# Kernel tuning notes

Hardware: AMD Instinct MI355X
Metric: run time of the kernel (lower is better)

Reference implementation:

```python
import jax, jax.numpy as jnp
import numpy as np

B, N, D, C = 256, 2000, 512, 100


def setup_inputs() -> dict:
    key = jax.random.key(0)
    k1, k2, k3, k4 = jax.random.split(key, 4)
    inputs = jax.random.normal(k1, (B, D), dtype=jnp.float32)
    support_tensors = jax.random.normal(k2, (N, D), dtype=jnp.float32)
    label_idx = jax.random.randint(k3, (N,), 0, C)
    support_labels = jax.nn.one_hot(label_idx, C, dtype=jnp.float32)
    kernel_w = jax.random.normal(k4, (D,), dtype=jnp.float32) * 0.05
    kernel_b = jnp.zeros((), dtype=jnp.float32)
    return {
        "inputs": inputs,
        "support_tensors": support_tensors,
        "support_labels": support_labels,
        "kernel_w": kernel_w,
        "kernel_b": kernel_b,
    }


def reference(inputs, support_tensors, support_labels, kernel_w, kernel_b):
    # Pairwise Cartesian product (batch x support): |a - b|, shape [B, N, D]
    diff = jnp.abs(inputs[:, None, :] - support_tensors[None, :, :])
    # Siamese kernel: sigmoid(Dense(1)(|a-b|)) -> scores [B, N]
    pair_wise_scores = jax.nn.sigmoid(jnp.einsum("bnd,d->bn", diff, kernel_w) + kernel_b)
    # Per-class aggregation: matmul with one-hot labels, then mean per class
    class_sums = pair_wise_scores @ support_labels  # [B, C]
    class_counts = jnp.sum(support_labels, axis=0)  # [C]
    # tf.math.divide_no_nan semantics
    return jnp.where(class_counts != 0, class_sums / class_counts, 0.0)
```

## Files before the change

kernel.cpp:

```cpp
#include <hip/hip_runtime.h>
#include <hip/hip_bf16.h>

#define B_SZ 256
#define N_SZ 2000
#define N_PAD 2048
#define D_SZ 512
#define C_SZ 100
#define BT 4
#define D4 (D_SZ / 4)
#define PF 4

__global__ void prep_kernel(const float* __restrict__ labels,
                            int* __restrict__ idx) {
    int n = blockIdx.x * 256 + threadIdx.x;
    if (n < N_SZ) {
        const float4* row = (const float4*)(labels + (size_t)n * C_SZ);
        int c = 0;
#pragma unroll
        for (int j = 0; j < C_SZ / 4; ++j) {
            float4 v = row[j];
            if (v.x > 0.5f) c = 4 * j + 0;
            if (v.y > 0.5f) c = 4 * j + 1;
            if (v.z > 0.5f) c = 4 * j + 2;
            if (v.w > 0.5f) c = 4 * j + 3;
        }
        idx[n] = c;
    }
}

__global__ void transpose_kernel(const float4* __restrict__ sup4,
                                 float4* __restrict__ supT4) {
    int t = blockIdx.x * 256 + threadIdx.x;
    int dc = t >> 11;
    int n  = t & (N_PAD - 1);
    float4 v = make_float4(0.f, 0.f, 0.f, 0.f);
    if (n < N_SZ) v = sup4[(size_t)n * D4 + dc];
    supT4[t] = v;
}

__global__ __launch_bounds__(256, 2) void score_kernel(
    const float4* __restrict__ inp4,
    const float4* __restrict__ supT4,
    const float4* __restrict__ w4,
    const float* __restrict__ bias_p,
    float* __restrict__ S)
{
    int tid = threadIdx.x;
    int n  = blockIdx.x * 256 + tid;
    int b0 = blockIdx.y * BT;

    const float4* __restrict__ a0 = inp4 + (size_t)(b0 + 0) * D4;
    const float4* __restrict__ a1 = inp4 + (size_t)(b0 + 1) * D4;
    const float4* __restrict__ a2 = inp4 + (size_t)(b0 + 2) * D4;
    const float4* __restrict__ a3 = inp4 + (size_t)(b0 + 3) * D4;

    const float4* __restrict__ sp = supT4 + n;

    float acc[BT] = {0.f, 0.f, 0.f, 0.f};

    auto compute = [&](int dc, const float4& sv) {
        float4 wv = w4[dc];
        float4 av;
        av = a0[dc];
        acc[0] += wv.x * fabsf(av.x - sv.x);
        acc[0] += wv.y * fabsf(av.y - sv.y);
        acc[0] += wv.z * fabsf(av.z - sv.z);
        acc[0] += wv.w * fabsf(av.w - sv.w);
        av = a1[dc];
        acc[1] += wv.x * fabsf(av.x - sv.x);
        acc[1] += wv.y * fabsf(av.y - sv.y);
        acc[1] += wv.z * fabsf(av.z - sv.z);
        acc[1] += wv.w * fabsf(av.w - sv.w);
        av = a2[dc];
        acc[2] += wv.x * fabsf(av.x - sv.x);
        acc[2] += wv.y * fabsf(av.y - sv.y);
        acc[2] += wv.z * fabsf(av.z - sv.z);
        acc[2] += wv.w * fabsf(av.w - sv.w);
        av = a3[dc];
        acc[3] += wv.x * fabsf(av.x - sv.x);
        acc[3] += wv.y * fabsf(av.y - sv.y);
        acc[3] += wv.z * fabsf(av.z - sv.z);
        acc[3] += wv.w * fabsf(av.w - sv.w);
    };

    float4 c0 = sp[(size_t)0 * N_PAD];
    float4 c1 = sp[(size_t)1 * N_PAD];
    float4 c2 = sp[(size_t)2 * N_PAD];
    float4 c3 = sp[(size_t)3 * N_PAD];

#pragma unroll 1
    for (int dc = 0; dc < D4 - PF; dc += PF) {
        float4 t0 = sp[(size_t)(dc + 4) * N_PAD];
        float4 t1 = sp[(size_t)(dc + 5) * N_PAD];
        float4 t2 = sp[(size_t)(dc + 6) * N_PAD];
        float4 t3 = sp[(size_t)(dc + 7) * N_PAD];
        compute(dc + 0, c0);
        compute(dc + 1, c1);
        compute(dc + 2, c2);
        compute(dc + 3, c3);
        c0 = t0; c1 = t1; c2 = t2; c3 = t3;
    }
    compute(D4 - 4, c0);
    compute(D4 - 3, c1);
    compute(D4 - 2, c2);
    compute(D4 - 1, c3);

    float bias = *bias_p;
#pragma unroll
    for (int i = 0; i < BT; ++i) {
        float s = 1.0f / (1.0f + __expf(-(acc[i] + bias)));
        S[(size_t)(b0 + i) * N_PAD + n] = s;
    }
}

__global__ void agg_kernel(const float* __restrict__ S,
                           const int* __restrict__ idx,
                           float* __restrict__ out) {
    __shared__ float sums[C_SZ];
    __shared__ float cnts[C_SZ];
    int b = blockIdx.x;
    int t = threadIdx.x;
    if (t < C_SZ) { sums[t] = 0.f; cnts[t] = 0.f; }
    __syncthreads();
    for (int n = t; n < N_SZ; n += 256) {
        int c = idx[n];
        atomicAdd(&sums[c], S[(size_t)b * N_PAD + n]);
        atomicAdd(&cnts[c], 1.0f);
    }
    __syncthreads();
    if (t < C_SZ) {
        float cnt = cnts[t];
        out[(size_t)b * C_SZ + t] = (cnt != 0.f) ? sums[t] / cnt : 0.f;
    }
}

extern "C" void kernel_launch(void* const* d_in, const int* in_sizes, int n_in,
                              void* d_out, int out_size, void* d_ws, size_t ws_size,
                              hipStream_t stream) {
    const float* inputs  = (const float*)d_in[0];
    const float* support = (const float*)d_in[1];
    const float* labels  = (const float*)d_in[2];
    const float* w       = (const float*)d_in[3];
    const float* bias    = (const float*)d_in[4];
    float* out = (float*)d_out;

    int*    idx   = (int*)d_ws;
    float4* supT4 = (float4*)((char*)d_ws + 16384);
    float*  S     = (float*)((char*)d_ws + 16384 + (size_t)D4 * N_PAD * sizeof(float4));

    prep_kernel<<<dim3((N_SZ + 255) / 256), dim3(256), 0, stream>>>(labels, idx);

    transpose_kernel<<<dim3(D4 * N_PAD / 256), dim3(256), 0, stream>>>(
        (const float4*)support, supT4);

    dim3 grid(N_PAD / 256, B_SZ / BT);
    score_kernel<<<grid, dim3(256), 0, stream>>>(
        (const float4*)inputs, supT4, (const float4*)w, bias, S);

    agg_kernel<<<dim3(B_SZ), dim3(256), 0, stream>>>(S, idx, out);
}
```

Baseline: 45.55 us.

## Split the D reduction across grid z and finish sigmoid in the aggregation kernel

The score kernel now splits the 512-wide feature reduction into four chunks along a third grid dimension. Each block writes partial logits to its own slice of the workspace, and the aggregation kernel adds the four partials plus the bias before applying the sigmoid. This multiplies the block count by four (from 512 blocks) and raises the launch-bounds occupancy hint, to fill the GPU better. In exchange it writes and reads four times as much intermediate data, and each block runs a much shorter loop with relatively more prologue overhead.

```diff
diff --git a/kernel.cpp b/kernel.cpp
--- a/kernel.cpp
+++ b/kernel.cpp
@@ -9,6 +9,8 @@
 #define BT 4
 #define D4 (D_SZ / 4)
 #define PF 4
+#define DSPLIT 4
+#define DQ (D4 / DSPLIT)
 
 __global__ void prep_kernel(const float* __restrict__ labels,
                             int* __restrict__ idx) {
@@ -38,28 +40,29 @@
     supT4[t] = v;
 }
 
-__global__ __launch_bounds__(256, 2) void score_kernel(
+__global__ __launch_bounds__(256, 8) void score_kernel(
     const float4* __restrict__ inp4,
     const float4* __restrict__ supT4,
     const float4* __restrict__ w4,
-    const float* __restrict__ bias_p,
     float* __restrict__ S)
 {
     int tid = threadIdx.x;
-    int n  = blockIdx.x * 256 + tid;
-    int b0 = blockIdx.y * BT;
+    int n   = blockIdx.x * 256 + tid;
+    int b0  = blockIdx.y * BT;
+    int off = blockIdx.z * DQ;
 
-    const float4* __restrict__ a0 = inp4 + (size_t)(b0 + 0) * D4;
-    const float4* __restrict__ a1 = inp4 + (size_t)(b0 + 1) * D4;
-    const float4* __restrict__ a2 = inp4 + (size_t)(b0 + 2) * D4;
-    const float4* __restrict__ a3 = inp4 + (size_t)(b0 + 3) * D4;
+    const float4* __restrict__ a0 = inp4 + (size_t)(b0 + 0) * D4 + off;
+    const float4* __restrict__ a1 = inp4 + (size_t)(b0 + 1) * D4 + off;
+    const float4* __restrict__ a2 = inp4 + (size_t)(b0 + 2) * D4 + off;
+    const float4* __restrict__ a3 = inp4 + (size_t)(b0 + 3) * D4 + off;
+    const float4* __restrict__ wq = w4 + off;
 
-    const float4* __restrict__ sp = supT4 + n;
+    const float4* __restrict__ sp = supT4 + (size_t)off * N_PAD + n;
 
     float acc[BT] = {0.f, 0.f, 0.f, 0.f};
 
     auto compute = [&](int dc, const float4& sv) {
-        float4 wv = w4[dc];
+        float4 wv = wq[dc];
         float4 av;
         av = a0[dc];
         acc[0] += wv.x * fabsf(av.x - sv.x);
@@ -89,7 +92,7 @@
     float4 c3 = sp[(size_t)3 * N_PAD];
 
 #pragma unroll 1
-    for (int dc = 0; dc < D4 - PF; dc += PF) {
+    for (int dc = 0; dc < DQ - PF; dc += PF) {
         float4 t0 = sp[(size_t)(dc + 4) * N_PAD];
         float4 t1 = sp[(size_t)(dc + 5) * N_PAD];
         float4 t2 = sp[(size_t)(dc + 6) * N_PAD];
@@ -100,21 +103,20 @@
         compute(dc + 3, c3);
         c0 = t0; c1 = t1; c2 = t2; c3 = t3;
     }
-    compute(D4 - 4, c0);
-    compute(D4 - 3, c1);
-    compute(D4 - 2, c2);
-    compute(D4 - 1, c3);
+    compute(DQ - 4, c0);
+    compute(DQ - 3, c1);
+    compute(DQ - 2, c2);
+    compute(DQ - 1, c3);
 
-    float bias = *bias_p;
+    float* __restrict__ Sz = S + ((size_t)blockIdx.z * B_SZ + b0) * N_PAD + n;
 #pragma unroll
-    for (int i = 0; i < BT; ++i) {
-        float s = 1.0f / (1.0f + __expf(-(acc[i] + bias)));
-        S[(size_t)(b0 + i) * N_PAD + n] = s;
-    }
+    for (int i = 0; i < BT; ++i)
+        Sz[(size_t)i * N_PAD] = acc[i];
 }
 
 __global__ void agg_kernel(const float* __restrict__ S,
                            const int* __restrict__ idx,
+                           const float* __restrict__ bias_p,
                            float* __restrict__ out) {
     __shared__ float sums[C_SZ];
     __shared__ float cnts[C_SZ];
@@ -122,9 +124,15 @@
     int t = threadIdx.x;
     if (t < C_SZ) { sums[t] = 0.f; cnts[t] = 0.f; }
     __syncthreads();
+    float bias = *bias_p;
     for (int n = t; n < N_SZ; n += 256) {
+        float logit = bias;
+#pragma unroll
+        for (int z = 0; z < DSPLIT; ++z)
+            logit += S[((size_t)z * B_SZ + b) * N_PAD + n];
+        float s = 1.0f / (1.0f + __expf(-logit));
         int c = idx[n];
-        atomicAdd(&sums[c], S[(size_t)b * N_PAD + n]);
+        atomicAdd(&sums[c], s);
         atomicAdd(&cnts[c], 1.0f);
     }
     __syncthreads();
@@ -153,9 +161,9 @@
     transpose_kernel<<<dim3(D4 * N_PAD / 256), dim3(256), 0, stream>>>(
         (const float4*)support, supT4);
 
-    dim3 grid(N_PAD / 256, B_SZ / BT);
+    dim3 grid(N_PAD / 256, B_SZ / BT, DSPLIT);
     score_kernel<<<grid, dim3(256), 0, stream>>>(
-        (const float4*)inputs, supT4, (const float4*)w, bias, S);
+        (const float4*)inputs, supT4, (const float4*)w, S);
 
-    agg_kernel<<<dim3(B_SZ), dim3(256), 0, stream>>>(S, idx, out);
+    agg_kernel<<<dim3(B_SZ), dim3(256), 0, stream>>>(S, idx, bias, out);
 }
```

New measurement: 49.64 us. +9.0%, slower.
